# Kernel tuning notes

Hardware: AMD Instinct MI355X
Metric: run time of the kernel (lower is better)

Reference implementation:

```python
import jax, jax.numpy as jnp
import numpy as np

N_NODES = 100000
N_EDGES = 1600000
EMBED_DIM = 64
NUM_HEADS = 4
HEAD_DIM = EMBED_DIM // NUM_HEADS  # 16


def mish(x):
    return x * jnp.tanh(jax.nn.softplus(x))


def setup_inputs() -> dict:
    key = jax.random.key(0)
    ks = jax.random.split(key, 8)
    x = jax.random.normal(ks[0], (N_NODES, EMBED_DIM), dtype=jnp.float32)
    senders = jax.random.randint(ks[1], (N_EDGES,), 0, N_NODES, dtype=jnp.int32)
    receivers = jax.random.randint(ks[2], (N_EDGES,), 0, N_NODES, dtype=jnp.int32)
    sc = 1.0 / np.sqrt(EMBED_DIM)
    # DenseGeneral(features=(H, d)) for senders / receivers, with bias
    Ws = jax.random.normal(ks[3], (EMBED_DIM, NUM_HEADS, HEAD_DIM), dtype=jnp.float32) * sc
    bs = jnp.zeros((NUM_HEADS, HEAD_DIM), dtype=jnp.float32)
    Wr = jax.random.normal(ks[4], (EMBED_DIM, NUM_HEADS, HEAD_DIM), dtype=jnp.float32) * sc
    br = jnp.zeros((NUM_HEADS, HEAD_DIM), dtype=jnp.float32)
    # Dense(1) on last axis (head_dim), weights shared across heads
    aw = jax.random.normal(ks[5], (HEAD_DIM,), dtype=jnp.float32) * (1.0 / np.sqrt(HEAD_DIM))
    ab = jnp.zeros((1,), dtype=jnp.float32)
    return {"x": x, "Ws": Ws, "bs": bs, "Wr": Wr, "br": br,
            "aw": aw, "ab": ab, "senders": senders, "receivers": receivers}


def reference(x, Ws, bs, Wr, br, aw, ab, senders, receivers):
    n = x.shape[0]
    # Node-level projections (same math as per-edge DenseGeneral, less traffic)
    s_proj = jnp.einsum('nf,fhd->nhd', x, Ws) + bs  # [N,H,d]
    r_proj = jnp.einsum('nf,fhd->nhd', x, Wr) + br  # [N,H,d]
    se = s_proj[senders]      # [E,H,d] gather of sender features
    re = r_proj[receivers]    # [E,H,d] gather of receiver features
    # GATv2 logit: Dense(1)(mish(s + r)) -> [E,H]
    logits = jnp.einsum('ehd,d->eh', mish(se + re), aw) + ab[0]
    # Segment softmax over incoming edges of each receiver node
    lmax = jax.ops.segment_max(logits, receivers, num_segments=n)
    ex = jnp.exp(logits - lmax[receivers])
    denom = jax.ops.segment_sum(ex, receivers, num_segments=n)
    alpha = ex / denom[receivers]  # [E,H]
    # Scatter-sum weighted sender features back to receiver nodes
    out = jax.ops.segment_sum(alpha[..., None] * se, receivers, num_segments=n)  # [N,H,d]
    return out.reshape(n, -1)  # [N, H*d]
```

## Files before the change

kernel.cpp:

```cpp
#include <hip/hip_runtime.h>
#include <hip/hip_fp16.h>
#include <math.h>

#define N_NODES 100000
#define N_EDGES 1600000
#define EMBED 64
#define HEADS 4
#define HDIM 16

#define SLOTS 64

#define BKT_SHIFT 8
#define BKT_NODES 256
#define NBKT 391
#define BKT_CAP 5120
#define TILE 4096
#define NTILE 391
#define NGRP (N_EDGES / 4)

#define NODES_BLK 64
#define NBLK_PROJ 1563
#define SMEM_BYTES 52224

#define LOG2E 1.44269504f

__device__ __forceinline__ float mish_aw(float z, float awc) {
    float ex  = __expf(fminf(z, 30.f));
    float u   = 1.f + ex;
    float den = fmaf(u, u, 1.f);
    float f   = fmaf(-2.f, __builtin_amdgcn_rcpf(den), 1.f);
    return z * awc * f;
}

template<int CTRL>
__device__ __forceinline__ float ror_add(float t) {
    int x = __builtin_amdgcn_mov_dpp(__float_as_int(t), CTRL, 0xF, 0xF, true);
    return t + __int_as_float(x);
}
__device__ __forceinline__ float head_reduce(float t) {
    t = ror_add<0x121>(t);
    t = ror_add<0x122>(t);
    t = ror_add<0x124>(t);
    t = ror_add<0x128>(t);
    return t;
}

template<int CTRL>
__device__ __forceinline__ __half2 hror_add(__half2 t) {
    int x = __builtin_amdgcn_mov_dpp(__builtin_bit_cast(int, t), CTRL, 0xF, 0xF, true);
    return __hadd2(t, __builtin_bit_cast(__half2, x));
}
__device__ __forceinline__ __half2 head_reduce_h2(__half2 t) {
    t = hror_add<0x121>(t);
    t = hror_add<0x122>(t);
    t = hror_add<0x124>(t);
    t = hror_add<0x128>(t);
    return t;
}

__global__ __launch_bounds__(256) void proj_bucketa_kernel(
        const float* __restrict__ x,
        const float* __restrict__ Ws, const float* __restrict__ bs,
        const float* __restrict__ Wr, const float* __restrict__ br,
        const int* __restrict__ senders, const int* __restrict__ receivers,
        unsigned short* __restrict__ sph, unsigned short* __restrict__ rph,
        int* __restrict__ bktcnt, int* __restrict__ bkt) {
    __shared__ __align__(16) char smem[SMEM_BYTES];
    int tid = threadIdx.x;
    if (blockIdx.x < NBLK_PROJ) {
        float* wsT = (float*)smem;
        float* wrT = wsT + 64 * 68;
        float* xsh = wrT + 64 * 68;
        for (int i = tid; i < 4096; i += 256) {
            int k = i >> 6, o = i & 63;
            wsT[o * 68 + k] = Ws[i];
            wrT[o * 68 + k] = Wr[i];
        }
        int nb = blockIdx.x * NODES_BLK;
        for (int i = 0; i < 4; ++i) {
            int g = i * 256 + tid;
            int nl = g >> 4;
            int k4 = g & 15;
            if (nb + nl < N_NODES) {
                float4 v = ((const float4*)(x + ((size_t)(nb + nl) << 6)))[k4];
                *(float4*)(xsh + nl * 68 + (k4 << 2)) = v;
            }
        }
        __syncthreads();
        int o = tid & 63;
        int w = tid >> 6;
        float bsv = bs[o], brv = br[o];
        float accs[16], accr[16];
#pragma unroll
        for (int p = 0; p < 16; ++p) { accs[p] = bsv; accr[p] = brv; }
        const float4* ws4 = (const float4*)wsT + o * 17;
        const float4* wr4 = (const float4*)wrT + o * 17;
        const float4* xs4 = (const float4*)xsh + (w << 4) * 17;
#pragma unroll 4
        for (int k4 = 0; k4 < 16; ++k4) {
            float4 a = ws4[k4];
            float4 b = wr4[k4];
#pragma unroll
            for (int p = 0; p < 16; ++p) {
                float4 xv = xs4[p * 17 + k4];
                accs[p] += xv.x * a.x + xv.y * a.y + xv.z * a.z + xv.w * a.w;
                accr[p] += xv.x * b.x + xv.y * b.y + xv.z * b.z + xv.w * b.w;
            }
        }
        int node0 = nb + (w << 4);
#pragma unroll
        for (int p = 0; p < 16; ++p) {
            int node = node0 + p;
            if (node < N_NODES) {
                sph[(node << 6) + o] = __half_as_ushort(__float2half_rn(accs[p]));
                rph[(node << 6) + o] = __half_as_ushort(__float2half_rn(accr[p]));
            }
        }
    } else {
        int* hist = (int*)smem;
        int* base = hist + NBKT;
        int* cur  = base + NBKT;
        for (int i = tid; i < NBKT; i += 256) hist[i] = 0;
        __syncthreads();
        int g0 = (blockIdx.x - NBLK_PROJ) * (TILE / 4);
        int4 r[4], s[4];
        bool v[4];
#pragma unroll
        for (int t = 0; t < 4; ++t) {
            int g = g0 + t * 256 + tid;
            v[t] = (g < NGRP);
            if (v[t]) {
                r[t] = ((const int4*)receivers)[g];
                s[t] = ((const int4*)senders)[g];
                atomicAdd(&hist[r[t].x >> BKT_SHIFT], 1);
                atomicAdd(&hist[r[t].y >> BKT_SHIFT], 1);
                atomicAdd(&hist[r[t].z >> BKT_SHIFT], 1);
                atomicAdd(&hist[r[t].w >> BKT_SHIFT], 1);
            }
        }
        __syncthreads();
        for (int i = tid; i < NBKT; i += 256) {
            int h = hist[i];
            base[i] = (h > 0) ? atomicAdd(&bktcnt[i], h) : 0;
            cur[i] = 0;
        }
        __syncthreads();
#pragma unroll
        for (int t = 0; t < 4; ++t) {
            if (v[t]) {
                int b, rk, slot;
                b = r[t].x >> BKT_SHIFT; rk = atomicAdd(&cur[b], 1); slot = base[b] + rk;
                if (slot < BKT_CAP) bkt[b * BKT_CAP + slot] = ((r[t].x & (BKT_NODES - 1)) << 17) | s[t].x;
                b = r[t].y >> BKT_SHIFT; rk = atomicAdd(&cur[b], 1); slot = base[b] + rk;
                if (slot < BKT_CAP) bkt[b * BKT_CAP + slot] = ((r[t].y & (BKT_NODES - 1)) << 17) | s[t].y;
                b = r[t].z >> BKT_SHIFT; rk = atomicAdd(&cur[b], 1); slot = base[b] + rk;
                if (slot < BKT_CAP) bkt[b * BKT_CAP + slot] = ((r[t].z & (BKT_NODES - 1)) << 17) | s[t].z;
                b = r[t].w >> BKT_SHIFT; rk = atomicAdd(&cur[b], 1); slot = base[b] + rk;
                if (slot < BKT_CAP) bkt[b * BKT_CAP + slot] = ((r[t].w & (BKT_NODES - 1)) << 17) | s[t].w;
            }
        }
    }
}

__global__ __launch_bounds__(1024) void bucketb_kernel(
        const int* __restrict__ bktcnt, const int* __restrict__ bkt,
        int* __restrict__ cursor, int* __restrict__ csr) {
    __shared__ int lcur[BKT_NODES];
    int tid = threadIdx.x;
    int b = blockIdx.x;
    if (tid < BKT_NODES) lcur[tid] = 0;
    __syncthreads();
    int cnt = bktcnt[b];
    if (cnt > BKT_CAP) cnt = BKT_CAP;
    const int* bb = bkt + b * BKT_CAP;
    for (int i = tid; i < cnt; i += 1024) {
        int vv = bb[i];
        int rl = vv >> 17;
        int sv = vv & 0x1FFFF;
        int slot = atomicAdd(&lcur[rl], 1);
        if (slot < SLOTS) csr[((((b << BKT_SHIFT) + rl)) << 6) + slot] = sv << 7;
    }
    __syncthreads();
    if (tid < BKT_NODES) {
        int node = (b << BKT_SHIFT) + tid;
        if (node < N_NODES) cursor[node] = lcur[tid];
    }
}

__global__ __launch_bounds__(256) void fused_gather_kernel(
                                    const unsigned short* __restrict__ sph,
                                    const unsigned short* __restrict__ rph,
                                    const int* __restrict__ csr,
                                    const int* __restrict__ cursor,
                                    const float* __restrict__ aw,
                                    const float* __restrict__ ab,
                                    float* __restrict__ out) {
    int wave = (blockIdx.x * blockDim.x + threadIdx.x) >> 6;
    wave = __builtin_amdgcn_readfirstlane(wave);
    int lane = threadIdx.x & 63;
    int deg = cursor[wave];
    deg = (deg > SLOTS) ? SLOTS : deg;
    const int* cbase = csr + (wave << 6);
    const char* splb = (const char*)sph + (lane << 1);
    float rp  = __half2float(__ushort_as_half(rph[(wave << 6) + lane]));
    float awc = aw[lane & 15];
    __half2 k_pk   = __float2half2_rn(LOG2E);
    __half2 rpk_pk = __float2half2_rn(rp * LOG2E);
    __half2 aw2_pk = __float2half2_rn(awc * LOG2E);
    __half2 rpa_pk = __float2half2_rn(rp * awc * LOG2E);
    __half2 ones   = __float2half2_rn(1.0f);
    __half2 neg2   = __float2half2_rn(-2.0f);
    __half2 l2a   = __float2half2_rn(0.0f), l2b   = __float2half2_rn(0.0f);
    __half2 acc2a = __float2half2_rn(0.0f), acc2b = __float2half2_rn(0.0f);
    float l_t = 0.f, acc_t = 0.f;
    int nb8 = deg >> 3;
    unsigned short cur[8], nxt[8];
    if (nb8 > 0) {
#pragma unroll
        for (int j = 0; j < 8; ++j) cur[j] = *(const unsigned short*)(splb + cbase[j]);
    }
    for (int k = 0; k < nb8; ++k) {
        if (k + 1 < nb8) {
            const int* cb = cbase + ((k + 1) << 3);
#pragma unroll
            for (int j = 0; j < 8; ++j) nxt[j] = *(const unsigned short*)(splb + cb[j]);
        }
#pragma unroll
        for (int j = 0; j < 4; ++j) {
            __half2 sp  = __halves2half2(__ushort_as_half(cur[2 * j]),
                                         __ushort_as_half(cur[2 * j + 1]));
            __half2 w   = h2exp2(__hfma2(sp, k_pk, rpk_pk));
            __half2 u   = __hadd2(w, ones);
            __half2 den = __hfma2(u, u, ones);
            __half2 r   = h2rcp(den);
            __half2 f   = __hfma2(neg2, r, ones);
            __half2 za  = __hfma2(sp, aw2_pk, rpa_pk);
            __half2 tt  = head_reduce_h2(__hmul2(za, f));
            __half2 p   = h2exp2(tt);
            if (j & 1) { l2b = __hadd2(l2b, p); acc2b = __hfma2(p, sp, acc2b); }
            else       { l2a = __hadd2(l2a, p); acc2a = __hfma2(p, sp, acc2a); }
        }
#pragma unroll
        for (int j = 0; j < 8; ++j) cur[j] = nxt[j];
    }
    int i = nb8 << 3;
    for (; i + 2 <= deg; i += 2) {
        __half2 sp  = __halves2half2(__ushort_as_half(*(const unsigned short*)(splb + cbase[i])),
                                     __ushort_as_half(*(const unsigned short*)(splb + cbase[i + 1])));
        __half2 w   = h2exp2(__hfma2(sp, k_pk, rpk_pk));
        __half2 u   = __hadd2(w, ones);
        __half2 den = __hfma2(u, u, ones);
        __half2 r   = h2rcp(den);
        __half2 f   = __hfma2(neg2, r, ones);
        __half2 za  = __hfma2(sp, aw2_pk, rpa_pk);
        __half2 tt  = head_reduce_h2(__hmul2(za, f));
        __half2 p   = h2exp2(tt);
        l2a   = __hadd2(l2a, p);
        acc2a = __hfma2(p, sp, acc2a);
    }
    if (i < deg) {
        float sp0 = __half2float(__ushort_as_half(*(const unsigned short*)(splb + cbase[i])));
        float t0 = head_reduce(mish_aw(sp0 + rp, awc));
        float p = __builtin_amdgcn_exp2f(t0 * LOG2E);
        l_t += p;
        acc_t = fmaf(p, sp0, acc_t);
    }
    __half2 l2   = __hadd2(l2a, l2b);
    __half2 acc2 = __hadd2(acc2a, acc2b);
    float l   = __low2float(l2) + __high2float(l2) + l_t;
    float acc = __low2float(acc2) + __high2float(acc2) + acc_t;
    out[(wave << 6) + lane] = (deg > 0) ? acc * __builtin_amdgcn_rcpf(l) : 0.f;
}

extern "C" void kernel_launch(void* const* d_in, const int* in_sizes, int n_in,
                              void* d_out, int out_size, void* d_ws, size_t ws_size,
                              hipStream_t stream) {
    const float* x  = (const float*)d_in[0];
    const float* Ws = (const float*)d_in[1];
    const float* bs = (const float*)d_in[2];
    const float* Wr = (const float*)d_in[3];
    const float* br = (const float*)d_in[4];
    const float* aw = (const float*)d_in[5];
    const float* ab = (const float*)d_in[6];
    const int* senders   = (const int*)d_in[7];
    const int* receivers = (const int*)d_in[8];
    float* out = (float*)d_out;

    char* wsp = (char*)d_ws;
    unsigned short* sph = (unsigned short*)wsp;  wsp += (size_t)N_NODES * EMBED * 2;
    unsigned short* rph = (unsigned short*)wsp;  wsp += (size_t)N_NODES * EMBED * 2;
    int* csr    = (int*)wsp;  wsp += (size_t)N_NODES * SLOTS * 4;
    int* cursor = (int*)wsp;  wsp += (size_t)N_NODES * 4;
    int* bkt    = (int*)wsp;  wsp += (size_t)NBKT * BKT_CAP * 4;
    int* bktcnt = (int*)wsp;  wsp += 512 * 4;

    hipMemsetAsync(bktcnt, 0, NBKT * 4, stream);

    proj_bucketa_kernel<<<NBLK_PROJ + NTILE, 256, 0, stream>>>(
        x, Ws, bs, Wr, br, senders, receivers, sph, rph, bktcnt, bkt);

    bucketb_kernel<<<NBKT, 1024, 0, stream>>>(bktcnt, bkt, cursor, csr);

    int gather_blocks = (N_NODES * 64 + 255) / 256;
    fused_gather_kernel<<<gather_blocks, 256, 0, stream>>>(sph, rph, csr, cursor,
                                                           aw, ab, out);
}
```

Before: 125.2 us.

## Replace global-atomic bucket allocation with per-tile fixed-capacity bucket segments

The bucketing phase stops reserving space in each receiver bucket through global atomics on a shared counter. Each edge tile now writes into its own fixed 32-slot segment per bucket and records a per-tile count, which removes the global atomics, the second local pass and the memset. The second kernel then walks every tile segment of its bucket and checks it against the stored counts. In exchange it reads a larger, sparsely filled buffer (391x391x32 ints), and edges beyond 32 per tile-bucket pair are silently dropped.

```diff
diff --git a/kernel.cpp b/kernel.cpp
--- a/kernel.cpp
+++ b/kernel.cpp
@@ -13,7 +13,7 @@
 #define BKT_SHIFT 8
 #define BKT_NODES 256
 #define NBKT 391
-#define BKT_CAP 5120
+#define CAP2 32
 #define TILE 4096
 #define NTILE 391
 #define NGRP (N_EDGES / 4)
@@ -64,7 +64,7 @@
         const float* __restrict__ Wr, const float* __restrict__ br,
         const int* __restrict__ senders, const int* __restrict__ receivers,
         unsigned short* __restrict__ sph, unsigned short* __restrict__ rph,
-        int* __restrict__ bktcnt, int* __restrict__ bkt) {
+        int* __restrict__ cnt2, int* __restrict__ bkt) {
     __shared__ __align__(16) char smem[SMEM_BYTES];
     int tid = threadIdx.x;
     if (blockIdx.x < NBLK_PROJ) {
@@ -117,68 +117,57 @@
             }
         }
     } else {
-        int* hist = (int*)smem;
-        int* base = hist + NBKT;
-        int* cur  = base + NBKT;
-        for (int i = tid; i < NBKT; i += 256) hist[i] = 0;
+        int* cur = (int*)smem;
+        for (int i = tid; i < NBKT; i += 256) cur[i] = 0;
         __syncthreads();
-        int g0 = (blockIdx.x - NBLK_PROJ) * (TILE / 4);
-        int4 r[4], s[4];
-        bool v[4];
+        int tile = blockIdx.x - NBLK_PROJ;
+        int g0 = tile * (TILE / 4);
 #pragma unroll
         for (int t = 0; t < 4; ++t) {
             int g = g0 + t * 256 + tid;
-            v[t] = (g < NGRP);
-            if (v[t]) {
-                r[t] = ((const int4*)receivers)[g];
-                s[t] = ((const int4*)senders)[g];
-                atomicAdd(&hist[r[t].x >> BKT_SHIFT], 1);
-                atomicAdd(&hist[r[t].y >> BKT_SHIFT], 1);
-                atomicAdd(&hist[r[t].z >> BKT_SHIFT], 1);
-                atomicAdd(&hist[r[t].w >> BKT_SHIFT], 1);
+            if (g < NGRP) {
+                int4 r = ((const int4*)receivers)[g];
+                int4 s = ((const int4*)senders)[g];
+                int b, rk;
+                b = r.x >> BKT_SHIFT; rk = atomicAdd(&cur[b], 1);
+                if (rk < CAP2) bkt[(b * NTILE + tile) * CAP2 + rk] = ((r.x & (BKT_NODES - 1)) << 17) | s.x;
+                b = r.y >> BKT_SHIFT; rk = atomicAdd(&cur[b], 1);
+                if (rk < CAP2) bkt[(b * NTILE + tile) * CAP2 + rk] = ((r.y & (BKT_NODES - 1)) << 17) | s.y;
+                b = r.z >> BKT_SHIFT; rk = atomicAdd(&cur[b], 1);
+                if (rk < CAP2) bkt[(b * NTILE + tile) * CAP2 + rk] = ((r.z & (BKT_NODES - 1)) << 17) | s.z;
+                b = r.w >> BKT_SHIFT; rk = atomicAdd(&cur[b], 1);
+                if (rk < CAP2) bkt[(b * NTILE + tile) * CAP2 + rk] = ((r.w & (BKT_NODES - 1)) << 17) | s.w;
             }
         }
         __syncthreads();
         for (int i = tid; i < NBKT; i += 256) {
-            int h = hist[i];
-            base[i] = (h > 0) ? atomicAdd(&bktcnt[i], h) : 0;
-            cur[i] = 0;
-        }
-        __syncthreads();
-#pragma unroll
-        for (int t = 0; t < 4; ++t) {
-            if (v[t]) {
-                int b, rk, slot;
-                b = r[t].x >> BKT_SHIFT; rk = atomicAdd(&cur[b], 1); slot = base[b] + rk;
-                if (slot < BKT_CAP) bkt[b * BKT_CAP + slot] = ((r[t].x & (BKT_NODES - 1)) << 17) | s[t].x;
-                b = r[t].y >> BKT_SHIFT; rk = atomicAdd(&cur[b], 1); slot = base[b] + rk;
-                if (slot < BKT_CAP) bkt[b * BKT_CAP + slot] = ((r[t].y & (BKT_NODES - 1)) << 17) | s[t].y;
-                b = r[t].z >> BKT_SHIFT; rk = atomicAdd(&cur[b], 1); slot = base[b] + rk;
-                if (slot < BKT_CAP) bkt[b * BKT_CAP + slot] = ((r[t].z & (BKT_NODES - 1)) << 17) | s[t].z;
-                b = r[t].w >> BKT_SHIFT; rk = atomicAdd(&cur[b], 1); slot = base[b] + rk;
-                if (slot < BKT_CAP) bkt[b * BKT_CAP + slot] = ((r[t].w & (BKT_NODES - 1)) << 17) | s[t].w;
-            }
+            int c = cur[i];
+            cnt2[i * NTILE + tile] = (c > CAP2) ? CAP2 : c;
         }
     }
 }
 
 __global__ __launch_bounds__(1024) void bucketb_kernel(
-        const int* __restrict__ bktcnt, const int* __restrict__ bkt,
+        const int* __restrict__ cnt2, const int* __restrict__ bkt,
         int* __restrict__ cursor, int* __restrict__ csr) {
+    __shared__ int scnt[NTILE];
     __shared__ int lcur[BKT_NODES];
     int tid = threadIdx.x;
     int b = blockIdx.x;
+    if (tid < NTILE) scnt[tid] = cnt2[b * NTILE + tid];
     if (tid < BKT_NODES) lcur[tid] = 0;
     __syncthreads();
-    int cnt = bktcnt[b];
-    if (cnt > BKT_CAP) cnt = BKT_CAP;
-    const int* bb = bkt + b * BKT_CAP;
-    for (int i = tid; i < cnt; i += 1024) {
-        int vv = bb[i];
-        int rl = vv >> 17;
-        int sv = vv & 0x1FFFF;
-        int slot = atomicAdd(&lcur[rl], 1);
-        if (slot < SLOTS) csr[((((b << BKT_SHIFT) + rl)) << 6) + slot] = sv << 7;
+    const int* bb = bkt + (size_t)b * NTILE * CAP2;
+    for (int i = tid; i < NTILE * CAP2; i += 1024) {
+        int seg = i >> 5;
+        int sl  = i & (CAP2 - 1);
+        if (sl < scnt[seg]) {
+            int vv = bb[i];
+            int rl = vv >> 17;
+            int sv = vv & 0x1FFFF;
+            int slot = atomicAdd(&lcur[rl], 1);
+            if (slot < SLOTS) csr[((((b << BKT_SHIFT) + rl)) << 6) + slot] = sv << 7;
+        }
     }
     __syncthreads();
     if (tid < BKT_NODES) {
@@ -291,15 +280,13 @@
     unsigned short* rph = (unsigned short*)wsp;  wsp += (size_t)N_NODES * EMBED * 2;
     int* csr    = (int*)wsp;  wsp += (size_t)N_NODES * SLOTS * 4;
     int* cursor = (int*)wsp;  wsp += (size_t)N_NODES * 4;
-    int* bkt    = (int*)wsp;  wsp += (size_t)NBKT * BKT_CAP * 4;
-    int* bktcnt = (int*)wsp;  wsp += 512 * 4;
-
-    hipMemsetAsync(bktcnt, 0, NBKT * 4, stream);
+    int* bkt    = (int*)wsp;  wsp += (size_t)NBKT * NTILE * CAP2 * 4;
+    int* cnt2   = (int*)wsp;  wsp += (size_t)NBKT * NTILE * 4;
 
     proj_bucketa_kernel<<<NBLK_PROJ + NTILE, 256, 0, stream>>>(
-        x, Ws, bs, Wr, br, senders, receivers, sph, rph, bktcnt, bkt);
-
-    bucketb_kernel<<<NBKT, 1024, 0, stream>>>(bktcnt, bkt, cursor, csr);
+        x, Ws, bs, Wr, br, senders, receivers, sph, rph, cnt2, bkt);
+
+    bucketb_kernel<<<NBKT, 1024, 0, stream>>>(cnt2, bkt, cursor, csr);
 
     int gather_blocks = (N_NODES * 64 + 255) / 256;
     fused_gather_kernel<<<gather_blocks, 256, 0, stream>>>(sph, rph, csr, cursor,
```

Measured after the change: 118.8 us. 1.05x faster.
